# Kernel tuning notes

Hardware: AMD Instinct MI355X
Metric: run time of the kernel (lower is better)

The kernel has to match this reference:

```python
import jax, jax.numpy as jnp
import numpy as np

B, S, HID = 1, 1024, 4096
NH, NKV, HD = 32, 8, 128
GROUPS = NH // NKV
THETA = 10000.0
SPAR = 0.5          # sparse_aggression (layer_idx > 0)
MIN_IDX = 4         # min_sparse_index: always-kept sink tokens
NEG = jnp.float32(-1e30)


def setup_inputs() -> dict:
    key = jax.random.key(0)
    k0, k1, k2, k3, k4 = jax.random.split(key, 5)
    sc = 0.02
    return {
        "hidden_states": jax.random.normal(k0, (B, S, HID), jnp.float32),
        "position_ids": jnp.arange(S, dtype=jnp.int32)[None, :],
        "Wq": jax.random.normal(k1, (NH * HD, HID), jnp.float32) * sc,
        "Wk": jax.random.normal(k2, (NKV * HD, HID), jnp.float32) * sc,
        "Wv": jax.random.normal(k3, (NKV * HD, HID), jnp.float32) * sc,
        "Wo": jax.random.normal(k4, (HID, NH * HD), jnp.float32) * sc,
    }


def _rotate_half(x):
    h = x.shape[-1] // 2
    return jnp.concatenate([-x[..., h:], x[..., :h]], axis=-1)


def _rope_cos_sin(position_ids):
    inv_freq = 1.0 / (THETA ** (jnp.arange(0, HD, 2, dtype=jnp.float32) / HD))
    freqs = position_ids.astype(jnp.float32)[..., None] * inv_freq  # [B,S,HD/2]
    emb = jnp.concatenate([freqs, freqs], axis=-1)                  # [B,S,HD]
    return jnp.cos(emb)[:, None], jnp.sin(emb)[:, None]             # [B,1,S,HD]


def reference(hidden_states, position_ids, Wq, Wk, Wv, Wo):
    b, s, _ = hidden_states.shape
    # QKV projections (nn.Linear: x @ W.T)
    q = (hidden_states @ Wq.T).reshape(b, s, NH, HD).transpose(0, 2, 1, 3)
    k = (hidden_states @ Wk.T).reshape(b, s, NKV, HD).transpose(0, 2, 1, 3)
    v = (hidden_states @ Wv.T).reshape(b, s, NKV, HD).transpose(0, 2, 1, 3)
    # RoPE
    cos, sin = _rope_cos_sin(position_ids)
    q = q * cos + _rotate_half(q) * sin
    k = k * cos + _rotate_half(k) * sin
    # repeat_kv (GQA expansion)
    k = jnp.repeat(k, GROUPS, axis=1)
    v = jnp.repeat(v, GROUPS, axis=1)
    # causal additive mask [1,1,S,S]
    causal = jnp.where(jnp.triu(jnp.ones((s, s), bool), 1), NEG, jnp.float32(0))[None, None]
    scale = 1.0 / np.sqrt(HD)
    scores = jnp.einsum('bhqd,bhkd->bhqk', q, k) * scale
    # oracle importance: softmax of (softmaxed) masked attention (no_grad in original)
    oracle = jax.nn.softmax((scores + causal).astype(jnp.float32), axis=-1)
    importance = jax.nn.softmax(oracle, axis=-1)
    importance = jax.lax.stop_gradient(importance)
    # descending sort -> rank of each key for each query
    sorted_idx = jnp.argsort(-importance, axis=-1)          # [B,H,S,S]
    ranks = jnp.argsort(sorted_idx, axis=-1)                # inverse perm
    # per-query token budget: keep ceil-ish top-k proportional to row length
    k_per_row = jnp.maximum((SPAR * (jnp.arange(s) + 1)).astype(jnp.int32), 1)
    key_idx = jnp.arange(s)
    kept = (ranks < k_per_row[None, None, :, None]) | (key_idx[None, None, None, :] < MIN_IDX)
    sparse_mask = jnp.where(kept, jnp.float32(0), NEG)
    # sparse attention
    attn = scores + sparse_mask + causal
    probs = jax.nn.softmax(attn.astype(jnp.float32), axis=-1).astype(v.dtype)
    out = jnp.einsum('bhqk,bhkd->bhqd', probs, v)           # [B,H,S,HD]
    out = out.transpose(0, 2, 1, 3).reshape(b, s, NH * HD)
    return out @ Wo.T
```

## Files before the change

### kernel.cpp

```cpp
#include <hip/hip_runtime.h>
#include <hip/hip_bf16.h>

#define S_LEN 1024
#define HID   4096
#define NH    32
#define NKV   8
#define HD    128
#define MIN_IDX 4
#define AO_COLS 4096
#define HEAD_STRIDE 131072

typedef __attribute__((ext_vector_type(8))) short short8;
typedef __attribute__((ext_vector_type(4))) float f32x4;

__device__ __forceinline__ unsigned short f2bf(float f) {
  union { float f; unsigned u; } v; v.f = f;
  unsigned r = v.u + 0x7FFFu + ((v.u >> 16) & 1u);
  return (unsigned short)(r >> 16);
}
__device__ __forceinline__ float bf2f(unsigned short h) {
  union { unsigned u; float f; } v; v.u = ((unsigned)h) << 16;
  return v.f;
}
__device__ __forceinline__ unsigned pk2(float a, float b) {
  union { __hip_bfloat162 h; unsigned u; } c;
  c.h = __float22bfloat162_rn(make_float2(a, b));
  return c.u;
}
__device__ __forceinline__ short8 pack8(float4 a, float4 b) {
  union { short8 s; unsigned u[4]; } r;
  r.u[0] = pk2(a.x, a.y); r.u[1] = pk2(a.z, a.w);
  r.u[2] = pk2(b.x, b.y); r.u[3] = pk2(b.z, b.w);
  return r.s;
}
__device__ __forceinline__ unsigned ordf(float f) {
  union { float f; int i; } v; v.f = f;
  return (unsigned)(v.i ^ ((v.i >> 31) | 0x80000000));
}
__device__ __forceinline__ float iordf(unsigned u) {
  union { int i; float f; } v;
  v.i = (u & 0x80000000u) ? (int)(u ^ 0x80000000u) : (int)~u;
  return v.f;
}
__device__ __forceinline__ float wave_sum_f(float v) {
  #pragma unroll
  for (int m = 32; m >= 1; m >>= 1) v += __shfl_xor(v, m);
  return v;
}
__device__ __forceinline__ unsigned wave_max_u(unsigned v) {
  #pragma unroll
  for (int m = 32; m >= 1; m >>= 1) { unsigned o = __shfl_xor(v, m); v = o > v ? o : v; }
  return v;
}
__device__ __forceinline__ void wave_lds_fence() {
  __builtin_amdgcn_s_waitcnt(0xC07F);
  __builtin_amdgcn_wave_barrier();
}
__device__ __forceinline__ void gload_lds16(const unsigned short* g, unsigned short* l) {
  auto gp = (const __attribute__((address_space(1))) unsigned*)g;
  auto lp = (__attribute__((address_space(3))) unsigned*)(unsigned)(unsigned long long)l;
  __builtin_amdgcn_global_load_lds(gp, lp, 16, 0, 0);
}

__global__ __launch_bounds__(256) void cvt_k(
    const float* __restrict__ src, unsigned short* __restrict__ dst)
{
  const size_t i = ((size_t)blockIdx.x * 256 + threadIdx.x) * 8;
  float4 a = *(const float4*)(src + i);
  float4 b = *(const float4*)(src + i + 4);
  *(short8*)(dst + i) = pack8(a, b);
}

__global__ __launch_bounds__(256) void cvt4_k(
    const float* __restrict__ s0, const float* __restrict__ s1,
    const float* __restrict__ s2, const float* __restrict__ s3,
    unsigned short* __restrict__ d0, unsigned short* __restrict__ d1)
{
  const int b = blockIdx.x;
  const float* src; unsigned short* dst; int rb;
  if (b < 2048)       { src = s0; dst = d0;            rb = b; }
  else if (b < 10240) { src = s1; dst = d1;            rb = b - 2048; }
  else if (b < 12288) { src = s2; dst = d1 + 16777216; rb = b - 10240; }
  else                { src = s3; dst = d1 + 20971520; rb = b - 12288; }
  const size_t i = ((size_t)rb * 256 + threadIdx.x) * 8;
  float4 a = *(const float4*)(src + i);
  float4 c = *(const float4*)(src + i + 4);
  *(short8*)(dst + i) = pack8(a, c);
}

__global__ __launch_bounds__(256) void gemm_qkv_k(
    const unsigned short* __restrict__ Xb, const unsigned short* __restrict__ Wb,
    unsigned short* __restrict__ Qraw, unsigned short* __restrict__ Kraw,
    unsigned short* __restrict__ Vt)
{
  __shared__ unsigned short As[3][128 * 32];
  __shared__ unsigned short Bs[3][128 * 32];
  const int nt = blockIdx.x;
  const int n0 = nt * 128;
  const int m0 = blockIdx.y * 128;
  const int t = threadIdx.x, w = t >> 6, lane = t & 63;
  const int wm = w >> 1, wn = w & 1;
  const int mcol = lane & 15, quad = lane >> 4;
  const int lrow = lane >> 2, lcol = (lane & 3) * 8;

  const unsigned short* Ag = Xb + (size_t)m0 * HID;
  const unsigned short* Bg = Wb + (size_t)n0 * HID;

  f32x4 acc[4][4];
  #pragma unroll
  for (int i = 0; i < 4; i++)
    #pragma unroll
    for (int j = 0; j < 4; j++) acc[i][j] = (f32x4){0.f, 0.f, 0.f, 0.f};

  constexpr int NT = HID / 32;
  #define STAGE_QKV(buf, k0)                                                  \
    { const int c0 = w * 2, c1 = w * 2 + 1;                                   \
      gload_lds16(Ag + (size_t)(c0*16 + lrow) * HID + (k0) + lcol, &As[buf][c0 * 512]); \
      gload_lds16(Bg + (size_t)(c0*16 + lrow) * HID + (k0) + lcol, &Bs[buf][c0 * 512]); \
      gload_lds16(Ag + (size_t)(c1*16 + lrow) * HID + (k0) + lcol, &As[buf][c1 * 512]); \
      gload_lds16(Bg + (size_t)(c1*16 + lrow) * HID + (k0) + lcol, &Bs[buf][c1 * 512]); }

  STAGE_QKV(0, 0)
  STAGE_QKV(1, 32)
  asm volatile("s_waitcnt vmcnt(4)" ::: "memory");
  __builtin_amdgcn_s_barrier();
  __builtin_amdgcn_sched_barrier(0);

  int cur = 0, stg = 2;
  for (int kt = 0; kt < NT; ++kt) {
    if (kt + 2 < NT) STAGE_QKV(stg, (kt + 2) * 32)
    short8 af[4], bf[4];
    #pragma unroll
    for (int i = 0; i < 4; i++) af[i] = *(const short8*)&As[cur][(wm*64 + i*16 + mcol)*32 + quad*8];
    #pragma unroll
    for (int j = 0; j < 4; j++) bf[j] = *(const short8*)&Bs[cur][(wn*64 + j*16 + mcol)*32 + quad*8];
    #pragma unroll
    for (int i = 0; i < 4; i++)
      #pragma unroll
      for (int j = 0; j < 4; j++)
        acc[i][j] = __builtin_amdgcn_mfma_f32_16x16x32_bf16(af[i], bf[j], acc[i][j], 0, 0, 0);
    if (kt + 2 < NT) { asm volatile("s_waitcnt vmcnt(4)" ::: "memory"); }
    else             { asm volatile("s_waitcnt vmcnt(0)" ::: "memory"); }
    __builtin_amdgcn_s_barrier();
    __builtin_amdgcn_sched_barrier(0);
    cur = (cur == 2) ? 0 : cur + 1;
    stg = (stg == 2) ? 0 : stg + 1;
  }

  if (nt < 40) {
    unsigned short* dst = (nt < 32) ? (Qraw + (size_t)nt * HEAD_STRIDE)
                                    : (Kraw + (size_t)(nt - 32) * HEAD_STRIDE);
    #pragma unroll
    for (int i = 0; i < 4; i++) {
      const int rb = m0 + wm*64 + i*16 + quad*4;
      #pragma unroll
      for (int j = 0; j < 4; j++) {
        const int d = wn*64 + j*16 + mcol;
        #pragma unroll
        for (int r = 0; r < 4; r++)
          dst[(size_t)(rb + r) * HD + d] = f2bf(acc[i][j][r]);
      }
    }
  } else {
    unsigned short* dst = Vt + (size_t)(nt - 40) * HEAD_STRIDE;
    #pragma unroll
    for (int i = 0; i < 4; i++) {
      const int rb = m0 + wm*64 + i*16 + quad*4;
      #pragma unroll
      for (int j = 0; j < 4; j++) {
        const int d = wn*64 + j*16 + mcol;
        ushort4 v4;
        v4.x = f2bf(acc[i][j][0]); v4.y = f2bf(acc[i][j][1]);
        v4.z = f2bf(acc[i][j][2]); v4.w = f2bf(acc[i][j][3]);
        *(ushort4*)(dst + (size_t)d * S_LEN + rb) = v4;
      }
    }
  }
}

__global__ __launch_bounds__(256) void rope_qk_k(
    const int* __restrict__ pos_ids,
    unsigned short* __restrict__ Qraw, unsigned short* __restrict__ Kraw)
{
  const int w = threadIdx.x >> 6, lane = threadIdx.x & 63;
  const int gw = blockIdx.x * 4 + w;
  const int hidx = gw >> 10;
  const int s = gw & 1023;
  const float pos = (float)pos_ids[s];
  const float invf = powf(10000.0f, -(float)lane * (1.0f / 64.0f));
  float sn, cs;
  sincosf(pos * invf, &sn, &cs);
  unsigned short* base = (hidx < NH)
      ? (Qraw + (size_t)hidx * HEAD_STRIDE + (size_t)s * HD)
      : (Kraw + (size_t)(hidx - NH) * HEAD_STRIDE + (size_t)s * HD);
  const float x0 = bf2f(base[lane]), x1 = bf2f(base[lane + 64]);
  base[lane]      = f2bf(x0 * cs - x1 * sn);
  base[lane + 64] = f2bf(x1 * cs + x0 * sn);
}

#define PSTR 1040
template<int KT>
__device__ __forceinline__ void attn_body(
    const unsigned short* __restrict__ Qb, const unsigned short* __restrict__ Kh,
    const unsigned short* __restrict__ Vh, unsigned short* __restrict__ AO,
    unsigned short (*Pl)[PSTR], unsigned (*hist)[256], float* rowinv,
    int q0, int h, int w, int lane, int mcol, int quad)
{
  constexpr int NC = 2 * KT;
  const float scale = 0.08838834764831845f;
  float (*scb)[16][130] = (float (*)[16][130])&Pl[0][0];

  short8 aq[4];
  {
    const unsigned short* qrow = Qb + ((size_t)h * S_LEN + q0 + mcol) * HD + quad * 8;
    #pragma unroll
    for (int kk = 0; kk < 4; kk++) aq[kk] = *(const short8*)(qrow + kk * 32);
  }

  unsigned su[4][NC];

  #pragma unroll
  for (int kt = 0; kt < KT; kt++) {
    short8 bfr[2][4];
    #pragma unroll
    for (int g2 = 0; g2 < 2; g2++) {
      const int key = kt * 128 + (w * 2 + g2) * 16 + mcol;
      const unsigned short* krow = Kh + (size_t)key * HD + quad * 8;
      #pragma unroll
      for (int kk = 0; kk < 4; kk++) bfr[g2][kk] = *(const short8*)(krow + kk * 32);
    }
    f32x4 d4[2];
    d4[0] = (f32x4){0.f,0.f,0.f,0.f}; d4[1] = (f32x4){0.f,0.f,0.f,0.f};
    #pragma unroll
    for (int g2 = 0; g2 < 2; g2++)
      #pragma unroll
      for (int kk = 0; kk < 4; kk++)
        d4[g2] = __builtin_amdgcn_mfma_f32_16x16x32_bf16(aq[kk], bfr[g2][kk], d4[g2], 0, 0, 0);
    #pragma unroll
    for (int g2 = 0; g2 < 2; g2++) {
      const int colc = (w * 2 + g2) * 16 + mcol;
      #pragma unroll
      for (int r = 0; r < 4; r++) scb[kt & 1][quad*4 + r][colc] = d4[g2][r] * scale;
    }
    __syncthreads();
    #pragma unroll
    for (int i = 0; i < 4; i++)
      #pragma unroll
      for (int sub = 0; sub < 2; sub++)
        su[i][kt*2 + sub] = ordf(scb[kt & 1][w*4 + i][sub*64 + lane]);
  }
  __syncthreads();

  const unsigned long long lmlt = (1ull << lane) - 1ull;
  const int rep = lane & 3;
  int Lr[4], krem[4], tot[4];
  unsigned prefix[4], pmsk[4];
  #pragma unroll
  for (int i = 0; i < 4; i++) {
    Lr[i] = q0 + w*4 + i + 1;
    int ks = Lr[i] >> 1; if (ks < 1) ks = 1;
    krem[i] = ks; tot[i] = Lr[i]; prefix[i] = 0u; pmsk[i] = 0u;
  }

  #pragma unroll
  for (int pass = 0; pass < 3; pass++) {
    const int shift = 26 - pass * 6;
    #pragma unroll
    for (int p = 0; p < 2; p++) {
      const int i0 = p*2, i1 = p*2 + 1;
      if (tot[i0] <= krem[i0] && tot[i1] <= krem[i1]) continue;
      { uint4 z = {0u, 0u, 0u, 0u}; *(uint4*)&hist[w][lane * 4] = z; }
      wave_lds_fence();
      #pragma unroll
      for (int c = 0; c < NC; c++) {
        const int j = c * 64 + lane;
        #pragma unroll
        for (int rr = 0; rr < 2; rr++) {
          const int i = p * 2 + rr;
          if (tot[i] > krem[i] && j < Lr[i] && (su[i][c] & pmsk[i]) == prefix[i])
            atomicAdd(&hist[w][((su[i][c] >> shift) & 63) * 4 + rep], 1u << (16 * rr));
        }
      }
      wave_lds_fence();
      const uint4 cv = *(const uint4*)&hist[w][(63 - lane) * 4];
      const unsigned cnt2 = cv.x + cv.y + cv.z + cv.w;
      unsigned x = cnt2;
      #pragma unroll
      for (int d2 = 1; d2 < 64; d2 <<= 1) { unsigned y = __shfl_up(x, d2); if (lane >= d2) x += y; }
      const unsigned runp = x - cnt2;
      #pragma unroll
      for (int rr = 0; rr < 2; rr++) {
        const int i = p * 2 + rr;
        if (tot[i] <= krem[i]) continue;
        const int sh16 = 16 * rr;
        const int run = (int)((runp >> sh16) & 0xFFFFu);
        const int cn  = (int)((cnt2 >> sh16) & 0xFFFFu);
        const bool hit = (run < krem[i]) && (run + cn >= krem[i]);
        unsigned packv = hit ? (((unsigned)(63 - lane) << 22) |
                                ((unsigned)run << 11) | (unsigned)cn) : 0u;
        const unsigned long long bal = __ballot(hit);
        const int srcl = __ffsll(bal) - 1;
        const unsigned res = __shfl(packv, srcl);
        const int bin = res >> 22;
        const int before = (res >> 11) & 0x7FF;
        const int cn2 = res & 0x7FF;
        krem[i] -= before;
        tot[i] = cn2;
        prefix[i] |= ((unsigned)bin) << shift;
        pmsk[i] |= 63u << shift;
      }
    }
  }

  #pragma unroll
  for (int i = 0; i < 4; i++) {
    const int r = w * 4 + i;
    const int L = Lr[i];
    unsigned btau = prefix[i];
    unsigned bmsk = pmsk[i];
    int kr = krem[i];
    int tt = tot[i];
    const int bs = (bmsk == 0u) ? 31 : (__builtin_ctz(bmsk) - 1);
    #pragma unroll 1
    for (int b = bs; b >= 0; --b) {
      if (tt <= kr) break;
      const unsigned bit = 1u << b;
      const unsigned am = bmsk | bit;
      const unsigned test = btau | bit;
      int cnt = 0;
      #pragma unroll
      for (int c = 0; c < NC; c++) {
        const int j = c * 64 + lane;
        cnt += (int)__popcll(__ballot(j < L && (su[i][c] & am) == test));
      }
      if (cnt >= kr) { btau = test; tt = cnt; }
      else           { kr -= cnt; tt -= cnt; }
      bmsk = am;
    }

    unsigned um = 0;
    #pragma unroll
    for (int c = 0; c < NC; c++) {
      const int j = c * 64 + lane;
      if (j < L && su[i][c] > um) um = su[i][c];
    }
    const float mx = iordf(wave_max_u(um));

    float ssum = 0.f;
    int tiebase = 0;
    #pragma unroll
    for (int c = 0; c < NC; c++) {
      const int j = c * 64 + lane;
      const unsigned u = su[i][c];
      const unsigned umv = u & bmsk;
      const bool eq = (j < L) && (umv == btau);
      const unsigned long long bal = __ballot(eq);
      const int trank = tiebase + (int)__popcll(bal & lmlt);
      tiebase += (int)__popcll(bal);
      const bool kept = (j < L) &&
          ((umv > btau) || (eq && trank < kr) || (j < MIN_IDX));
      const float e = kept ? __expf(iordf(u) - mx) : 0.f;
      Pl[r][c*64 + lane] = f2bf(e);
      ssum += e;
    }
    ssum = wave_sum_f(ssum);
    if (lane == 0) rowinv[r] = 1.f / fmaxf(ssum, 1e-30f);
  }
  __syncthreads();

  f32x4 opv[2];
  opv[0] = (f32x4){0.f,0.f,0.f,0.f}; opv[1] = (f32x4){0.f,0.f,0.f,0.f};
  #pragma unroll
  for (int kt = 0; kt < KT; kt++) {
    #pragma unroll
    for (int kb = 0; kb < 4; kb++) {
      short8 af = *(const short8*)&Pl[mcol][kt*128 + kb*32 + quad*8];
      #pragma unroll
      for (int n2 = 0; n2 < 2; n2++) {
        const int d = (w*2 + n2) * 16 + mcol;
        short8 bfr = *(const short8*)(Vh + (size_t)d * S_LEN + kt*128 + kb*32 + quad*8);
        opv[n2] = __builtin_amdgcn_mfma_f32_16x16x32_bf16(af, bfr, opv[n2], 0, 0, 0);
      }
    }
  }
  #pragma unroll
  for (int n2 = 0; n2 < 2; n2++) {
    const int col = h * HD + (w*2 + n2) * 16 + mcol;
    #pragma unroll
    for (int r2 = 0; r2 < 4; r2++) {
      const int row = q0 + quad*4 + r2;
      AO[(size_t)row * AO_COLS + col] = f2bf(opv[n2][r2] * rowinv[quad*4 + r2]);
    }
  }
}

__global__ __launch_bounds__(256, 4) void attn_k(
    const unsigned short* __restrict__ Qb, const unsigned short* __restrict__ Kb,
    const unsigned short* __restrict__ Vt, unsigned short* __restrict__ AO)
{
  __shared__ unsigned short Pl[16][PSTR];
  __shared__ unsigned hist[4][256];
  __shared__ float rowinv[16];
  const int rb = (int)gridDim.x - 1 - (int)blockIdx.x;
  const int h = blockIdx.y;
  const int kvh = h >> 2;
  const int q0 = rb * 16;
  const int kt_max = (rb >> 3) + 1;
  const int t = threadIdx.x, w = t >> 6, lane = t & 63;
  const int mcol = lane & 15, quad = lane >> 4;
  const unsigned short* Kh = Kb + (size_t)kvh * HEAD_STRIDE;
  const unsigned short* Vh = Vt + (size_t)kvh * HEAD_STRIDE;

  switch (kt_max) {
    case 1: attn_body<1>(Qb, Kh, Vh, AO, Pl, hist, rowinv, q0, h, w, lane, mcol, quad); break;
    case 2: attn_body<2>(Qb, Kh, Vh, AO, Pl, hist, rowinv, q0, h, w, lane, mcol, quad); break;
    case 3: attn_body<3>(Qb, Kh, Vh, AO, Pl, hist, rowinv, q0, h, w, lane, mcol, quad); break;
    case 4: attn_body<4>(Qb, Kh, Vh, AO, Pl, hist, rowinv, q0, h, w, lane, mcol, quad); break;
    case 5: attn_body<5>(Qb, Kh, Vh, AO, Pl, hist, rowinv, q0, h, w, lane, mcol, quad); break;
    case 6: attn_body<6>(Qb, Kh, Vh, AO, Pl, hist, rowinv, q0, h, w, lane, mcol, quad); break;
    case 7: attn_body<7>(Qb, Kh, Vh, AO, Pl, hist, rowinv, q0, h, w, lane, mcol, quad); break;
    default: attn_body<8>(Qb, Kh, Vh, AO, Pl, hist, rowinv, q0, h, w, lane, mcol, quad); break;
  }
}

__global__ __launch_bounds__(256) void gemm_out_k(
    const unsigned short* __restrict__ A, const unsigned short* __restrict__ Wob,
    float* __restrict__ Out)
{
  __shared__ unsigned short As[3][128 * 32];
  __shared__ unsigned short Bs[3][128 * 32];
  const int n0 = blockIdx.x * 128;
  const int m0 = blockIdx.y * 128;
  const int t = threadIdx.x, w = t >> 6, lane = t & 63;
  const int wm = w >> 1, wn = w & 1;
  const int mcol = lane & 15, quad = lane >> 4;
  const int lrow = lane >> 2, lcol = (lane & 3) * 8;

  const unsigned short* Ag = A   + (size_t)m0 * AO_COLS;
  const unsigned short* Bg = Wob + (size_t)n0 * AO_COLS;

  f32x4 acc[4][4];
  #pragma unroll
  for (int i = 0; i < 4; i++)
    #pragma unroll
    for (int j = 0; j < 4; j++) acc[i][j] = (f32x4){0.f, 0.f, 0.f, 0.f};

  constexpr int NT = AO_COLS / 32;
  #define STAGE_OUT(buf, k0)                                                  \
    { const int c0 = w * 2, c1 = w * 2 + 1;                                   \
      gload_lds16(Ag + (size_t)(c0*16 + lrow) * AO_COLS + (k0) + lcol, &As[buf][c0 * 512]); \
      gload_lds16(Bg + (size_t)(c0*16 + lrow) * AO_COLS + (k0) + lcol, &Bs[buf][c0 * 512]); \
      gload_lds16(Ag + (size_t)(c1*16 + lrow) * AO_COLS + (k0) + lcol, &As[buf][c1 * 512]); \
      gload_lds16(Bg + (size_t)(c1*16 + lrow) * AO_COLS + (k0) + lcol, &Bs[buf][c1 * 512]); }

  STAGE_OUT(0, 0)
  STAGE_OUT(1, 32)
  asm volatile("s_waitcnt vmcnt(4)" ::: "memory");
  __builtin_amdgcn_s_barrier();
  __builtin_amdgcn_sched_barrier(0);

  int cur = 0, stg = 2;
  for (int kt = 0; kt < NT; ++kt) {
    if (kt + 2 < NT) STAGE_OUT(stg, (kt + 2) * 32)
    short8 af[4], bf[4];
    #pragma unroll
    for (int i = 0; i < 4; i++) af[i] = *(const short8*)&As[cur][(wm*64 + i*16 + mcol)*32 + quad*8];
    #pragma unroll
    for (int j = 0; j < 4; j++) bf[j] = *(const short8*)&Bs[cur][(wn*64 + j*16 + mcol)*32 + quad*8];
    #pragma unroll
    for (int i = 0; i < 4; i++)
      #pragma unroll
      for (int j = 0; j < 4; j++)
        acc[i][j] = __builtin_amdgcn_mfma_f32_16x16x32_bf16(af[i], bf[j], acc[i][j], 0, 0, 0);
    if (kt + 2 < NT) { asm volatile("s_waitcnt vmcnt(4)" ::: "memory"); }
    else             { asm volatile("s_waitcnt vmcnt(0)" ::: "memory"); }
    __builtin_amdgcn_s_barrier();
    __builtin_amdgcn_sched_barrier(0);
    cur = (cur == 2) ? 0 : cur + 1;
    stg = (stg == 2) ? 0 : stg + 1;
  }

  #pragma unroll
  for (int i = 0; i < 4; i++) {
    const int rb = m0 + wm*64 + i*16 + quad*4;
    #pragma unroll
    for (int j = 0; j < 4; j++) {
      const int col = n0 + wn*64 + j*16 + mcol;
      #pragma unroll
      for (int r = 0; r < 4; r++)
        Out[(size_t)(rb + r) * HID + col] = acc[i][j][r];
    }
  }
}

extern "C" void kernel_launch(void* const* d_in, const int* in_sizes, int n_in,
                              void* d_out, int out_size, void* d_ws, size_t ws_size,
                              hipStream_t stream) {
  (void)in_sizes; (void)n_in; (void)out_size; (void)ws_size;
  const float* X   = (const float*)d_in[0];
  const int*   pos = (const int*)d_in[1];
  const float* Wq  = (const float*)d_in[2];
  const float* Wk  = (const float*)d_in[3];
  const float* Wv  = (const float*)d_in[4];
  const float* Wo  = (const float*)d_in[5];
  float* out = (float*)d_out;

  char* ws = (char*)d_ws;
  unsigned short* Qraw  = (unsigned short*)ws;
  unsigned short* Kraw  = (unsigned short*)(ws + 8388608);
  unsigned short* Vt    = (unsigned short*)(ws + 10485760);
  unsigned short* AO    = (unsigned short*)(ws + 12582912);
  unsigned short* Xb    = (unsigned short*)(ws + 20971520);
  unsigned short* Wqkvb = (unsigned short*)(ws + 29360128);
  unsigned short* Wob   = Wqkvb;

  cvt4_k<<<dim3(14336), dim3(256), 0, stream>>>(X, Wq, Wk, Wv, Xb, Wqkvb);

  gemm_qkv_k<<<dim3(48, 8),  dim3(256), 0, stream>>>(Xb, Wqkvb, Qraw, Kraw, Vt);
  rope_qk_k <<<dim3(10240),  dim3(256), 0, stream>>>(pos, Qraw, Kraw);

  cvt_k<<<dim3(8192), dim3(256), 0, stream>>>(Wo, Wob);

  attn_k    <<<dim3(64, 32), dim3(256), 0, stream>>>(Qraw, Kraw, Vt, AO);
  gemm_out_k<<<dim3(32, 8),  dim3(256), 0, stream>>>(AO, Wob, out);
}
```

Baseline: 456.4 us.

## Stage full score rows in LDS and process two rows at a time

The attention kernel now writes all QK scores for the 16-row tile into a float LDS buffer in one pass, removing the per-tile barrier. Register-resident scores are cut from four rows to two rows per wave, with the radix select and softmax done per row pair. This lowers register pressure and barrier count, but LDS grows to about 66KB, so launch bounds drop from 4 to 2 blocks per CU, which risks lower occupancy. RoPE's powf is also replaced by exp2f.

```diff
diff --git a/kernel.cpp b/kernel.cpp
--- a/kernel.cpp
+++ b/kernel.cpp
@@ -187,7 +187,7 @@
   const int hidx = gw >> 10;
   const int s = gw & 1023;
   const float pos = (float)pos_ids[s];
-  const float invf = powf(10000.0f, -(float)lane * (1.0f / 64.0f));
+  const float invf = exp2f((float)lane * -0.20762050593045f);
   float sn, cs;
   sincosf(pos * invf, &sn, &cs);
   unsigned short* base = (hidx < NH)
@@ -198,17 +198,72 @@
   base[lane + 64] = f2bf(x1 * cs + x0 * sn);
 }
 
-#define PSTR 1040
+#define SROW 1042
+#define PSTR 2084
+
+#define PROC_ROW(UARR, RR, LL, PRE, PM, KRM, TTT)                             \
+  {                                                                           \
+    const int r_ = (RR);                                                      \
+    const int L_ = (LL);                                                      \
+    unsigned btau = (PRE);                                                    \
+    unsigned bmsk = (PM);                                                     \
+    int kr = (KRM);                                                           \
+    int tt = (TTT);                                                           \
+    const int bs = (bmsk == 0u) ? 31 : (__builtin_ctz(bmsk) - 1);             \
+    _Pragma("unroll 1")                                                       \
+    for (int b = bs; b >= 0; --b) {                                           \
+      if (tt <= kr) break;                                                    \
+      const unsigned bit = 1u << b;                                           \
+      const unsigned am = bmsk | bit;                                         \
+      const unsigned test = btau | bit;                                       \
+      int cnt = 0;                                                            \
+      _Pragma("unroll")                                                       \
+      for (int c = 0; c < NC; c++) {                                          \
+        const int j = c * 64 + lane;                                          \
+        cnt += (int)__popcll(__ballot(j < L_ && ((UARR)[c] & am) == test));   \
+      }                                                                       \
+      if (cnt >= kr) { btau = test; tt = cnt; }                               \
+      else           { kr -= cnt; tt -= cnt; }                                \
+      bmsk = am;                                                              \
+    }                                                                         \
+    unsigned um = 0;                                                          \
+    _Pragma("unroll")                                                         \
+    for (int c = 0; c < NC; c++) {                                            \
+      const int j = c * 64 + lane;                                            \
+      if (j < L_ && (UARR)[c] > um) um = (UARR)[c];                           \
+    }                                                                         \
+    const float mx = iordf(wave_max_u(um));                                   \
+    float ssum = 0.f;                                                         \
+    int tiebase = 0;                                                          \
+    _Pragma("unroll")                                                         \
+    for (int c = 0; c < NC; c++) {                                            \
+      const int j = c * 64 + lane;                                            \
+      const unsigned u = (UARR)[c];                                           \
+      const unsigned umv = u & bmsk;                                          \
+      const bool eq = (j < L_) && (umv == btau);                              \
+      const unsigned long long bal = __ballot(eq);                            \
+      const int trank = tiebase + (int)__popcll(bal & lmlt);                  \
+      tiebase += (int)__popcll(bal);                                          \
+      const bool kept = (j < L_) &&                                           \
+          ((umv > btau) || (eq && trank < kr) || (j < MIN_IDX));              \
+      const float e = kept ? __expf(iordf(u) - mx) : 0.f;                     \
+      Pl[r_][c*64 + lane] = f2bf(e);                                          \
+      ssum += e;                                                              \
+    }                                                                         \
+    ssum = wave_sum_f(ssum);                                                  \
+    if (lane == 0) rowinv[r_] = 1.f / fmaxf(ssum, 1e-30f);                    \
+  }
+
 template<int KT>
 __device__ __forceinline__ void attn_body(
     const unsigned short* __restrict__ Qb, const unsigned short* __restrict__ Kh,
     const unsigned short* __restrict__ Vh, unsigned short* __restrict__ AO,
-    unsigned short (*Pl)[PSTR], unsigned (*hist)[256], float* rowinv,
+    float (*S)[SROW], unsigned (*hist)[256], float* rowinv,
     int q0, int h, int w, int lane, int mcol, int quad)
 {
   constexpr int NC = 2 * KT;
   const float scale = 0.08838834764831845f;
-  float (*scb)[16][130] = (float (*)[16][130])&Pl[0][0];
+  unsigned short (*Pl)[PSTR] = (unsigned short (*)[PSTR])&S[0][0];
 
   short8 aq[4];
   {
@@ -217,8 +272,6 @@
     for (int kk = 0; kk < 4; kk++) aq[kk] = *(const short8*)(qrow + kk * 32);
   }
 
-  unsigned su[4][NC];
-
   #pragma unroll
   for (int kt = 0; kt < KT; kt++) {
     short8 bfr[2][4];
@@ -238,48 +291,44 @@
         d4[g2] = __builtin_amdgcn_mfma_f32_16x16x32_bf16(aq[kk], bfr[g2][kk], d4[g2], 0, 0, 0);
     #pragma unroll
     for (int g2 = 0; g2 < 2; g2++) {
-      const int colc = (w * 2 + g2) * 16 + mcol;
-      #pragma unroll
-      for (int r = 0; r < 4; r++) scb[kt & 1][quad*4 + r][colc] = d4[g2][r] * scale;
-    }
-    __syncthreads();
-    #pragma unroll
-    for (int i = 0; i < 4; i++)
-      #pragma unroll
-      for (int sub = 0; sub < 2; sub++)
-        su[i][kt*2 + sub] = ordf(scb[kt & 1][w*4 + i][sub*64 + lane]);
+      const int ckey = kt * 128 + (w * 2 + g2) * 16 + mcol;
+      #pragma unroll
+      for (int r = 0; r < 4; r++) S[quad*4 + r][ckey] = d4[g2][r] * scale;
+    }
   }
   __syncthreads();
 
   const unsigned long long lmlt = (1ull << lane) - 1ull;
   const int rep = lane & 3;
-  int Lr[4], krem[4], tot[4];
-  unsigned prefix[4], pmsk[4];
-  #pragma unroll
-  for (int i = 0; i < 4; i++) {
-    Lr[i] = q0 + w*4 + i + 1;
-    int ks = Lr[i] >> 1; if (ks < 1) ks = 1;
-    krem[i] = ks; tot[i] = Lr[i]; prefix[i] = 0u; pmsk[i] = 0u;
-  }
-
-  #pragma unroll
-  for (int pass = 0; pass < 3; pass++) {
-    const int shift = 26 - pass * 6;
-    #pragma unroll
-    for (int p = 0; p < 2; p++) {
-      const int i0 = p*2, i1 = p*2 + 1;
-      if (tot[i0] <= krem[i0] && tot[i1] <= krem[i1]) continue;
+  #pragma unroll
+  for (int p = 0; p < 2; p++) {
+    const int ra = w*4 + p*2, rbn = ra + 1;
+    const int L0 = q0 + ra + 1, L1 = q0 + rbn + 1;
+    unsigned u0[NC], u1[NC];
+    #pragma unroll
+    for (int c = 0; c < NC; c++) {
+      u0[c] = ordf(S[ra][c*64 + lane]);
+      u1[c] = ordf(S[rbn][c*64 + lane]);
+    }
+    int ks0 = L0 >> 1; if (ks0 < 1) ks0 = 1;
+    int ks1 = L1 >> 1; if (ks1 < 1) ks1 = 1;
+    int krem0 = ks0, tot0 = L0, krem1 = ks1, tot1 = L1;
+    unsigned pre0 = 0u, pre1 = 0u, pm0 = 0u, pm1 = 0u;
+
+    #pragma unroll
+    for (int pass = 0; pass < 3; pass++) {
+      const int shift = 26 - pass * 6;
+      const bool a0 = tot0 > krem0, a1 = tot1 > krem1;
+      if (!a0 && !a1) continue;
       { uint4 z = {0u, 0u, 0u, 0u}; *(uint4*)&hist[w][lane * 4] = z; }
       wave_lds_fence();
       #pragma unroll
       for (int c = 0; c < NC; c++) {
         const int j = c * 64 + lane;
-        #pragma unroll
-        for (int rr = 0; rr < 2; rr++) {
-          const int i = p * 2 + rr;
-          if (tot[i] > krem[i] && j < Lr[i] && (su[i][c] & pmsk[i]) == prefix[i])
-            atomicAdd(&hist[w][((su[i][c] >> shift) & 63) * 4 + rep], 1u << (16 * rr));
-        }
+        if (a0 && j < L0 && (u0[c] & pm0) == pre0)
+          atomicAdd(&hist[w][((u0[c] >> shift) & 63) * 4 + rep], 1u);
+        if (a1 && j < L1 && (u1[c] & pm1) == pre1)
+          atomicAdd(&hist[w][((u1[c] >> shift) & 63) * 4 + rep], 1u << 16);
       }
       wave_lds_fence();
       const uint4 cv = *(const uint4*)&hist[w][(63 - lane) * 4];
@@ -288,83 +337,37 @@
       #pragma unroll
       for (int d2 = 1; d2 < 64; d2 <<= 1) { unsigned y = __shfl_up(x, d2); if (lane >= d2) x += y; }
       const unsigned runp = x - cnt2;
-      #pragma unroll
-      for (int rr = 0; rr < 2; rr++) {
-        const int i = p * 2 + rr;
-        if (tot[i] <= krem[i]) continue;
-        const int sh16 = 16 * rr;
-        const int run = (int)((runp >> sh16) & 0xFFFFu);
-        const int cn  = (int)((cnt2 >> sh16) & 0xFFFFu);
-        const bool hit = (run < krem[i]) && (run + cn >= krem[i]);
+      if (a0) {
+        const int run = (int)(runp & 0xFFFFu);
+        const int cn  = (int)(cnt2 & 0xFFFFu);
+        const bool hit = (run < krem0) && (run + cn >= krem0);
         unsigned packv = hit ? (((unsigned)(63 - lane) << 22) |
                                 ((unsigned)run << 11) | (unsigned)cn) : 0u;
         const unsigned long long bal = __ballot(hit);
         const int srcl = __ffsll(bal) - 1;
         const unsigned res = __shfl(packv, srcl);
-        const int bin = res >> 22;
-        const int before = (res >> 11) & 0x7FF;
-        const int cn2 = res & 0x7FF;
-        krem[i] -= before;
-        tot[i] = cn2;
-        prefix[i] |= ((unsigned)bin) << shift;
-        pmsk[i] |= 63u << shift;
+        krem0 -= (int)((res >> 11) & 0x7FF);
+        tot0 = (int)(res & 0x7FF);
+        pre0 |= ((unsigned)(res >> 22)) << shift;
+        pm0 |= 63u << shift;
       }
-    }
-  }
-
-  #pragma unroll
-  for (int i = 0; i < 4; i++) {
-    const int r = w * 4 + i;
-    const int L = Lr[i];
-    unsigned btau = prefix[i];
-    unsigned bmsk = pmsk[i];
-    int kr = krem[i];
-    int tt = tot[i];
-    const int bs = (bmsk == 0u) ? 31 : (__builtin_ctz(bmsk) - 1);
-    #pragma unroll 1
-    for (int b = bs; b >= 0; --b) {
-      if (tt <= kr) break;
-      const unsigned bit = 1u << b;
-      const unsigned am = bmsk | bit;
-      const unsigned test = btau | bit;
-      int cnt = 0;
-      #pragma unroll
-      for (int c = 0; c < NC; c++) {
-        const int j = c * 64 + lane;
-        cnt += (int)__popcll(__ballot(j < L && (su[i][c] & am) == test));
+      if (a1) {
+        const int run = (int)(runp >> 16);
+        const int cn  = (int)(cnt2 >> 16);
+        const bool hit = (run < krem1) && (run + cn >= krem1);
+        unsigned packv = hit ? (((unsigned)(63 - lane) << 22) |
+                                ((unsigned)run << 11) | (unsigned)cn) : 0u;
+        const unsigned long long bal = __ballot(hit);
+        const int srcl = __ffsll(bal) - 1;
+        const unsigned res = __shfl(packv, srcl);
+        krem1 -= (int)((res >> 11) & 0x7FF);
+        tot1 = (int)(res & 0x7FF);
+        pre1 |= ((unsigned)(res >> 22)) << shift;
+        pm1 |= 63u << shift;
       }
-      if (cnt >= kr) { btau = test; tt = cnt; }
-      else           { kr -= cnt; tt -= cnt; }
-      bmsk = am;
-    }
-
-    unsigned um = 0;
-    #pragma unroll
-    for (int c = 0; c < NC; c++) {
-      const int j = c * 64 + lane;
-      if (j < L && su[i][c] > um) um = su[i][c];
-    }
-    const float mx = iordf(wave_max_u(um));
-
-    float ssum = 0.f;
-    int tiebase = 0;
-    #pragma unroll
-    for (int c = 0; c < NC; c++) {
-      const int j = c * 64 + lane;
-      const unsigned u = su[i][c];
-      const unsigned umv = u & bmsk;
-      const bool eq = (j < L) && (umv == btau);
-      const unsigned long long bal = __ballot(eq);
-      const int trank = tiebase + (int)__popcll(bal & lmlt);
-      tiebase += (int)__popcll(bal);
-      const bool kept = (j < L) &&
-          ((umv > btau) || (eq && trank < kr) || (j < MIN_IDX));
-      const float e = kept ? __expf(iordf(u) - mx) : 0.f;
-      Pl[r][c*64 + lane] = f2bf(e);
-      ssum += e;
-    }
-    ssum = wave_sum_f(ssum);
-    if (lane == 0) rowinv[r] = 1.f / fmaxf(ssum, 1e-30f);
+    }
+    PROC_ROW(u0, ra,  L0, pre0, pm0, krem0, tot0)
+    PROC_ROW(u1, rbn, L1, pre1, pm1, krem1, tot1)
   }
   __syncthreads();
 
@@ -394,11 +397,11 @@
   }
 }
 
-__global__ __launch_bounds__(256, 4) void attn_k(
+__global__ __launch_bounds__(256, 2) void attn_k(
     const unsigned short* __restrict__ Qb, const unsigned short* __restrict__ Kb,
     const unsigned short* __restrict__ Vt, unsigned short* __restrict__ AO)
 {
-  __shared__ unsigned short Pl[16][PSTR];
+  __shared__ float S[16][SROW];
   __shared__ unsigned hist[4][256];
   __shared__ float rowinv[16];
   const int rb = (int)gridDim.x - 1 - (int)blockIdx.x;
@@ -412,14 +415,14 @@
   const unsigned short* Vh = Vt + (size_t)kvh * HEAD_STRIDE;
 
   switch (kt_max) {
-    case 1: attn_body<1>(Qb, Kh, Vh, AO, Pl, hist, rowinv, q0, h, w, lane, mcol, quad); break;
-    case 2: attn_body<2>(Qb, Kh, Vh, AO, Pl, hist, rowinv, q0, h, w, lane, mcol, quad); break;
-    case 3: attn_body<3>(Qb, Kh, Vh, AO, Pl, hist, rowinv, q0, h, w, lane, mcol, quad); break;
-    case 4: attn_body<4>(Qb, Kh, Vh, AO, Pl, hist, rowinv, q0, h, w, lane, mcol, quad); break;
-    case 5: attn_body<5>(Qb, Kh, Vh, AO, Pl, hist, rowinv, q0, h, w, lane, mcol, quad); break;
-    case 6: attn_body<6>(Qb, Kh, Vh, AO, Pl, hist, rowinv, q0, h, w, lane, mcol, quad); break;
-    case 7: attn_body<7>(Qb, Kh, Vh, AO, Pl, hist, rowinv, q0, h, w, lane, mcol, quad); break;
-    default: attn_body<8>(Qb, Kh, Vh, AO, Pl, hist, rowinv, q0, h, w, lane, mcol, quad); break;
+    case 1: attn_body<1>(Qb, Kh, Vh, AO, S, hist, rowinv, q0, h, w, lane, mcol, quad); break;
+    case 2: attn_body<2>(Qb, Kh, Vh, AO, S, hist, rowinv, q0, h, w, lane, mcol, quad); break;
+    case 3: attn_body<3>(Qb, Kh, Vh, AO, S, hist, rowinv, q0, h, w, lane, mcol, quad); break;
+    case 4: attn_body<4>(Qb, Kh, Vh, AO, S, hist, rowinv, q0, h, w, lane, mcol, quad); break;
+    case 5: attn_body<5>(Qb, Kh, Vh, AO, S, hist, rowinv, q0, h, w, lane, mcol, quad); break;
+    case 6: attn_body<6>(Qb, Kh, Vh, AO, S, hist, rowinv, q0, h, w, lane, mcol, quad); break;
+    case 7: attn_body<7>(Qb, Kh, Vh, AO, S, hist, rowinv, q0, h, w, lane, mcol, quad); break;
+    default: attn_body<8>(Qb, Kh, Vh, AO, S, hist, rowinv, q0, h, w, lane, mcol, quad); break;
   }
 }
 
```

New measurement: 468.9 us. +2.7%, slower.
